# Kernel tuning notes

Measured on AMD Instinct MI355X. Metric: run time of the kernel, lower is better.

The kernel has to match this reference:

```python
import jax, jax.numpy as jnp
import numpy as np

# RT-DETR multi-scale deformable attention reference (PPMSDeformableAttention forward, value_mask=None)
SPATIAL_SHAPES = ((80, 80), (40, 40), (20, 20))  # (H, W) per level; sum(H*W) = 8400 = Len_v
NUM_HEADS = 8
NUM_LEVELS = 3
NUM_POINTS = 4


def _gather_corner(v_l, ix, iy, H, W):
    # v_l: [bs, heads, H*W, hd]; ix/iy: [bs, heads, N] int32 pixel indices (possibly out of range)
    valid = (ix >= 0) & (ix < W) & (iy >= 0) & (iy < H)
    idx = jnp.clip(iy, 0, H - 1) * W + jnp.clip(ix, 0, W - 1)
    g = jnp.take_along_axis(v_l, idx[..., None], axis=2)  # [bs, heads, N, hd]
    return jnp.where(valid[..., None], g, jnp.zeros((), v_l.dtype))


def _bilinear_sample(v_l, px, py, H, W):
    # grid_sample(align_corners=False, padding_mode='zeros') semantics.
    # v_l: [bs, heads, H*W, hd]; px/py: [bs, heads, N] continuous pixel coords
    x0 = jnp.floor(px).astype(jnp.int32)
    y0 = jnp.floor(py).astype(jnp.int32)
    x1, y1 = x0 + 1, y0 + 1
    wx1 = px - x0.astype(px.dtype)
    wy1 = py - y0.astype(py.dtype)
    wx0, wy0 = 1.0 - wx1, 1.0 - wy1
    out = (_gather_corner(v_l, x0, y0, H, W) * (wx0 * wy0)[..., None]
           + _gather_corner(v_l, x1, y0, H, W) * (wx1 * wy0)[..., None]
           + _gather_corner(v_l, x0, y1, H, W) * (wx0 * wy1)[..., None]
           + _gather_corner(v_l, x1, y1, H, W) * (wx1 * wy1)[..., None])
    return out  # [bs, heads, N, hd]


def setup_inputs() -> dict:
    key = jax.random.key(0)
    ks = jax.random.split(key, 8)
    bs, Lq, C = 32, 300, 256
    Lv = sum(h * w for h, w in SPATIAL_SHAPES)
    tp = NUM_HEADS * NUM_LEVELS * NUM_POINTS  # 96
    s = 1.0 / np.sqrt(C)
    return {
        "query": jax.random.normal(ks[0], (bs, Lq, C), jnp.float32),
        "reference_points": jax.random.uniform(ks[1], (bs, Lq, NUM_LEVELS, 4), jnp.float32, 0.05, 0.95),
        "value": jax.random.normal(ks[2], (bs, Lv, C), jnp.float32),
        "Wv": jax.random.normal(ks[3], (C, C), jnp.float32) * s,
        "bv": jnp.zeros((C,), jnp.float32),
        "Woff": jax.random.normal(ks[4], (C, tp * 2), jnp.float32) * (s * 0.1),
        "boff": jax.random.normal(ks[5], (tp * 2,), jnp.float32) * 0.5,
        "Watt": jax.random.normal(ks[6], (C, tp), jnp.float32) * s,
        "batt": jnp.zeros((tp,), jnp.float32),
        "Wout": jax.random.normal(ks[7], (C, C), jnp.float32) * s,
        "bout": jnp.zeros((C,), jnp.float32),
    }


def reference(query, reference_points, value, Wv, bv, Woff, boff, Watt, batt, Wout, bout):
    bs, Lq, C = query.shape
    H_, L, P = NUM_HEADS, NUM_LEVELS, NUM_POINTS
    hd = C // H_
    Lv = value.shape[1]

    # value projection -> [bs, heads, Lv, hd]
    v = (value @ Wv + bv).reshape(bs, Lv, H_, hd).transpose(0, 2, 1, 3)

    # sampling offsets and attention weights from query
    off = (query @ Woff + boff).reshape(bs, Lq, H_, L, P, 2)
    attw = jax.nn.softmax((query @ Watt + batt).reshape(bs, Lq, H_, L * P), axis=-1)
    attw = attw.reshape(bs, Lq, H_, L, P)

    # reference_points last dim == 4: (cx, cy, w, h) normalized
    ref_xy = reference_points[:, :, None, :, None, :2]  # [bs,Lq,1,L,1,2]
    ref_wh = reference_points[:, :, None, :, None, 2:]
    loc = ref_xy + off / P * ref_wh * 0.5  # [bs,Lq,H,L,P,2], normalized [0,1]

    out = jnp.zeros((bs, Lq, H_, hd), query.dtype)
    start = 0
    for l, (H, W) in enumerate(SPATIAL_SHAPES):
        v_l = v[:, :, start:start + H * W]  # [bs, heads, H*W, hd]
        start += H * W
        # normalized -> pixel coords (align_corners=False): p = loc * size - 0.5
        locl = loc[:, :, :, l]  # [bs, Lq, heads, P, 2]
        px = locl[..., 0] * W - 0.5
        py = locl[..., 1] * H - 0.5
        # [bs, Lq, heads, P] -> [bs, heads, Lq*P]
        px = px.transpose(0, 2, 1, 3).reshape(bs, H_, Lq * P)
        py = py.transpose(0, 2, 1, 3).reshape(bs, H_, Lq * P)
        sampled = _bilinear_sample(v_l, px, py, H, W)  # [bs, heads, Lq*P, hd]
        sampled = sampled.reshape(bs, H_, Lq, P, hd)
        out = out + jnp.einsum('bhqpd,bqhp->bqhd', sampled, attw[:, :, :, l])

    out = out.reshape(bs, Lq, C)
    return out @ Wout + bout
```

## Files before the change

### kernel.cpp

```cpp
#include <hip/hip_runtime.h>
#include <hip/hip_bf16.h>

#define BS 32
#define LQ 300
#define CDIM 256
#define HEADS 8
#define HD 32
#define NLEVELS 3
#define NPOINTS 4
#define LV 8400
#define NOA 288

typedef __attribute__((ext_vector_type(4))) float f32x4;
typedef __attribute__((ext_vector_type(8))) short short8;
typedef __attribute__((ext_vector_type(8))) unsigned short u16x8;
typedef __attribute__((ext_vector_type(4))) unsigned short u16x4;

__device__ __forceinline__ unsigned short f2bf(float f) {
    __hip_bfloat16 h = __float2bfloat16(f);
    return __bfloat16_as_ushort(h);
}
__device__ __forceinline__ float bf2f(unsigned short u) {
    union { unsigned u; float f; } v; v.u = ((unsigned)u) << 16;
    return v.f;
}

__global__ void prep_weights_kernel(
    const float* __restrict__ Wv, const float* __restrict__ Wout,
    const float* __restrict__ Woff, const float* __restrict__ Watt,
    unsigned short* __restrict__ WvT, unsigned short* __restrict__ WoutT,
    unsigned short* __restrict__ WoaT)
{
    const int bid = blockIdx.x;
    const int k = threadIdx.x;
    if (bid < 256) {
        WvT[bid * 256 + k] = f2bf(Wv[k * 256 + bid]);
    } else if (bid < 512) {
        const int n = bid - 256;
        WoutT[n * 256 + k] = f2bf(Wout[k * 256 + n]);
    } else {
        const int n = bid - 512;
        const float w = (n < 192) ? Woff[k * 192 + n] : Watt[k * 96 + (n - 192)];
        WoaT[n * 256 + k] = f2bf(w);
    }
}

#define BM 128
#define BK 32
#define PAD 40
#define EPAD 264
#define NT (CDIM / BK)

__global__ __launch_bounds__(512) void proj_value_mfma(
    const float* __restrict__ value, const unsigned short* __restrict__ WvT,
    const float* __restrict__ bv, unsigned short* __restrict__ vout)
{
    __shared__ alignas(16) unsigned short lds_w[2][256 * PAD];
    __shared__ alignas(16) unsigned short lds_x[2][128 * PAD];
    unsigned short* lds_ep = &lds_w[0][0];

    const int tid = threadIdx.x;
    const int lane = tid & 63;
    const int wave = tid >> 6;
    const int wm = wave >> 2;
    const int wn = wave & 3;
    const long row0 = (long)blockIdx.x * BM;

    const int wr = tid >> 1, wk = (tid & 1) * 16;
    const unsigned short* wptr = WvT + (size_t)wr * CDIM + wk;
    const int xr = tid >> 2, xk = (tid & 3) * 8;
    const float* xptr = value + (row0 + xr) * CDIM + xk;

    u16x8 wrg[2];
    f32x4 xrg[2];

    auto load_tile = [&](int kb) {
        const u16x8* qw = (const u16x8*)(wptr + kb);
        wrg[0] = qw[0]; wrg[1] = qw[1];
        const float* p = xptr + kb;
        xrg[0] = *(const f32x4*)(p);
        xrg[1] = *(const f32x4*)(p + 4);
    };
    auto write_tile = [&](int buf) {
        u16x8* ww = (u16x8*)&lds_w[buf][wr * PAD + wk];
        ww[0] = wrg[0]; ww[1] = wrg[1];
        u16x8 t0;
#pragma unroll
        for (int i = 0; i < 4; ++i) {
            t0[i]     = f2bf(xrg[0][i]);
            t0[i + 4] = f2bf(xrg[1][i]);
        }
        *(u16x8*)&lds_x[buf][xr * PAD + xk] = t0;
    };

    f32x4 acc[4][4] = {};
    const int la = lane & 15;
    const int lg = lane >> 4;

    load_tile(0);
    write_tile(0);
    __syncthreads();
    int cur = 0;

    for (int t = 0; t < NT; ++t) {
        if (t + 1 < NT) load_tile((t + 1) * BK);

        const unsigned short* pw = &lds_w[cur][(wn * 64 + la) * PAD + lg * 8];
        const unsigned short* px = &lds_x[cur][(wm * 64 + la) * PAD + lg * 8];
        short8 xf[4];
#pragma unroll
        for (int mf = 0; mf < 4; ++mf)
            xf[mf] = *(const short8*)(px + mf * 16 * PAD);
#pragma unroll
        for (int nf = 0; nf < 4; ++nf) {
            const short8 wf = *(const short8*)(pw + nf * 16 * PAD);
#pragma unroll
            for (int mf = 0; mf < 4; ++mf)
                acc[nf][mf] = __builtin_amdgcn_mfma_f32_16x16x32_bf16(wf, xf[mf], acc[nf][mf], 0, 0, 0);
        }

        if (t + 1 < NT) write_tile(cur ^ 1);
        __syncthreads();
        cur ^= 1;
    }

#pragma unroll
    for (int pass = 0; pass < 2; ++pass) {
        __syncthreads();
        if (wm == pass) {
#pragma unroll
            for (int nf = 0; nf < 4; ++nf) {
                const int nbase = wn * 64 + nf * 16 + lg * 4;
                const f32x4 bb = *(const f32x4*)&bv[nbase];
#pragma unroll
                for (int mf = 0; mf < 4; ++mf) {
                    const int mloc = mf * 16 + la;
                    u16x4 o;
#pragma unroll
                    for (int j = 0; j < 4; ++j) o[j] = f2bf(acc[nf][mf][j] + bb[j]);
                    *(u16x4*)&lds_ep[mloc * EPAD + nbase] = o;
                }
            }
        }
        __syncthreads();
        const int er = tid >> 3;
        const int ec = (tid & 7) * 32;
        const long gr = row0 + pass * 64 + er;
        const u16x8* src = (const u16x8*)&lds_ep[er * EPAD + ec];
        u16x8* dst = (u16x8*)&vout[gr * CDIM + ec];
#pragma unroll
        for (int i = 0; i < 4; ++i) dst[i] = src[i];
    }
}

#define APAD 40
#define BPAD 40

__global__ __launch_bounds__(256) void offatt_gemm_mfma(
    const float* __restrict__ query, const unsigned short* __restrict__ WoaT,
    const float* __restrict__ boff, const float* __restrict__ batt,
    float* __restrict__ offatt)
{
    __shared__ unsigned short lds_a[2][BM * APAD];
    __shared__ unsigned short lds_b[2][NOA * BPAD];

    const int tid = threadIdx.x;
    const int lane = tid & 63;
    const int wave = tid >> 6;
    const int wm = wave >> 1;
    const int wn = wave & 1;
    const long row0 = (long)blockIdx.x * BM;

    const int ar = tid >> 1;
    const int ak = (tid & 1) * 16;
    const float* aptr = query + (row0 + ar) * CDIM + ak;
    const unsigned short* bptr  = WoaT + (size_t)tid * CDIM;
    const unsigned short* bptr2 = WoaT + (size_t)(256 + tid) * CDIM;
    const bool extra = tid < 32;

    f32x4 arg[4];
    u16x8 brg[4], brg2[4];

    auto load_tile = [&](int kb) {
        const float* p = aptr + kb;
        arg[0] = *(const f32x4*)(p);
        arg[1] = *(const f32x4*)(p + 4);
        arg[2] = *(const f32x4*)(p + 8);
        arg[3] = *(const f32x4*)(p + 12);
        const u16x8* q = (const u16x8*)(bptr + kb);
        brg[0] = q[0]; brg[1] = q[1]; brg[2] = q[2]; brg[3] = q[3];
        if (extra) {
            const u16x8* q2 = (const u16x8*)(bptr2 + kb);
            brg2[0] = q2[0]; brg2[1] = q2[1]; brg2[2] = q2[2]; brg2[3] = q2[3];
        }
    };
    auto write_tile = [&](int buf) {
        u16x8 t0, t1;
#pragma unroll
        for (int i = 0; i < 4; ++i) {
            t0[i]     = f2bf(arg[0][i]);
            t0[i + 4] = f2bf(arg[1][i]);
            t1[i]     = f2bf(arg[2][i]);
            t1[i + 4] = f2bf(arg[3][i]);
        }
        u16x8* wa = (u16x8*)&lds_a[buf][ar * APAD + ak];
        wa[0] = t0; wa[1] = t1;
        u16x8* wb = (u16x8*)&lds_b[buf][tid * BPAD];
        wb[0] = brg[0]; wb[1] = brg[1]; wb[2] = brg[2]; wb[3] = brg[3];
        if (extra) {
            u16x8* wb2 = (u16x8*)&lds_b[buf][(256 + tid) * BPAD];
            wb2[0] = brg2[0]; wb2[1] = brg2[1]; wb2[2] = brg2[2]; wb2[3] = brg2[3];
        }
    };

    f32x4 acc[4][9] = {};
    const int la = lane & 15;
    const int lg = lane >> 4;

    load_tile(0);
    write_tile(0);
    __syncthreads();
    int cur = 0;

    for (int t = 0; t < CDIM / BK; ++t) {
        if (t + 1 < CDIM / BK) load_tile((t + 1) * BK);

        const unsigned short* pa = &lds_a[cur][(wm * 64 + la) * APAD + lg * 8];
        const unsigned short* pb = &lds_b[cur][(wn * 144 + la) * BPAD + lg * 8];
        short8 af[4];
#pragma unroll
        for (int mi = 0; mi < 4; ++mi)
            af[mi] = *(const short8*)(pa + mi * 16 * APAD);
#pragma unroll
        for (int ni = 0; ni < 9; ++ni) {
            const short8 bf = *(const short8*)(pb + ni * 16 * BPAD);
#pragma unroll
            for (int mi = 0; mi < 4; ++mi)
                acc[mi][ni] = __builtin_amdgcn_mfma_f32_16x16x32_bf16(af[mi], bf, acc[mi][ni], 0, 0, 0);
        }

        if (t + 1 < CDIM / BK) write_tile(cur ^ 1);
        __syncthreads();
        cur ^= 1;
    }

    float bias[9];
#pragma unroll
    for (int ni = 0; ni < 9; ++ni) {
        const int col = wn * 144 + ni * 16 + la;
        bias[ni] = (col < 192) ? boff[col] : batt[col - 192];
    }
#pragma unroll
    for (int mi = 0; mi < 4; ++mi) {
#pragma unroll
        for (int ni = 0; ni < 9; ++ni) {
            const int col = wn * 144 + ni * 16 + la;
#pragma unroll
            for (int j = 0; j < 4; ++j) {
                const long r = row0 + wm * 64 + mi * 16 + lg * 4 + j;
                offatt[r * NOA + col] = acc[mi][ni][j] + bias[ni];
            }
        }
    }
}

__global__ __launch_bounds__(256) void sample_kernel(
    const float* __restrict__ offatt, const float* __restrict__ refpts,
    const unsigned short* __restrict__ v, unsigned short* __restrict__ mid)
{
    __shared__ float oa_s[NOA];
    __shared__ float aw_s[96];
    __shared__ float px_s[96];
    __shared__ float py_s[96];

    const int tid = threadIdx.x;
    const int b = blockIdx.x / LQ;
    const int q = blockIdx.x % LQ;
    const long bq = (long)b * LQ + q;

    oa_s[tid] = offatt[bq * NOA + tid];
    if (tid < 32) oa_s[256 + tid] = offatt[bq * NOA + 256 + tid];
    __syncthreads();

    if (tid < 8) {
        float m = -1e30f;
#pragma unroll
        for (int i = 0; i < 12; ++i) m = fmaxf(m, oa_s[192 + tid * 12 + i]);
        float e[12];
        float s = 0.f;
#pragma unroll
        for (int i = 0; i < 12; ++i) { e[i] = __expf(oa_s[192 + tid * 12 + i] - m); s += e[i]; }
        const float inv = 1.f / s;
#pragma unroll
        for (int i = 0; i < 12; ++i) aw_s[tid * 12 + i] = e[i] * inv;
    }
    if (tid >= 128 && tid < 224) {
        const int t = tid - 128;
        const int h = t / 12, idx = t % 12, l = idx >> 2, p = idx & 3;
        const float* rp = refpts + (bq * NLEVELS + l) * 4;
        const float rx = rp[0], ry = rp[1], rw = rp[2], rh = rp[3];
        const float ox = oa_s[((h * NLEVELS + l) * NPOINTS + p) * 2 + 0];
        const float oy = oa_s[((h * NLEVELS + l) * NPOINTS + p) * 2 + 1];
        const float lx = rx + ox * 0.125f * rw;
        const float ly = ry + oy * 0.125f * rh;
        const int Wl = 80 >> l;
        px_s[t] = lx * (float)Wl - 0.5f;
        py_s[t] = ly * (float)Wl - 0.5f;
    }
    __syncthreads();

    const int h = tid >> 5;
    const int pg = (tid >> 3) & 3;
    const int d4 = tid & 7;
    const unsigned short* vb = v + ((size_t)b * LV) * CDIM + h * HD + d4 * 4;

    float a0 = 0.f, a1 = 0.f, a2 = 0.f, a3 = 0.f;
#pragma unroll
    for (int j = 0; j < 3; ++j) {
        const int i = pg * 3 + j;
        const int l = i >> 2;
        const int idx = h * 12 + i;
        const float px = px_s[idx], py = py_s[idx], aw = aw_s[idx];
        const int Wl = 80 >> l;
        const int start = (l == 0) ? 0 : (l == 1) ? 6400 : 8000;

        const float fx = floorf(px), fy = floorf(py);
        const int x0 = (int)fx, y0 = (int)fy;
        const float wx1 = px - fx, wy1 = py - fy;
        const float wx0 = 1.f - wx1, wy0 = 1.f - wy1;
        const float w00 = wx0 * wy0 * aw, w10 = wx1 * wy0 * aw;
        const float w01 = wx0 * wy1 * aw, w11 = wx1 * wy1 * aw;
        const bool x0v = (unsigned)x0 < (unsigned)Wl;
        const bool x1v = (unsigned)(x0 + 1) < (unsigned)Wl;
        const bool y0v = (unsigned)y0 < (unsigned)Wl;
        const bool y1v = (unsigned)(y0 + 1) < (unsigned)Wl;

        const unsigned short* base = vb + (size_t)start * CDIM;
        if (y0v) {
            const unsigned short* r0p = base + (size_t)(y0 * Wl) * CDIM;
            if (x0v) {
                const u16x4 u = *(const u16x4*)(r0p + (size_t)x0 * CDIM);
                a0 = fmaf(w00, bf2f(u[0]), a0); a1 = fmaf(w00, bf2f(u[1]), a1);
                a2 = fmaf(w00, bf2f(u[2]), a2); a3 = fmaf(w00, bf2f(u[3]), a3);
            }
            if (x1v) {
                const u16x4 u = *(const u16x4*)(r0p + (size_t)(x0 + 1) * CDIM);
                a0 = fmaf(w10, bf2f(u[0]), a0); a1 = fmaf(w10, bf2f(u[1]), a1);
                a2 = fmaf(w10, bf2f(u[2]), a2); a3 = fmaf(w10, bf2f(u[3]), a3);
            }
        }
        if (y1v) {
            const unsigned short* r1p = base + (size_t)((y0 + 1) * Wl) * CDIM;
            if (x0v) {
                const u16x4 u = *(const u16x4*)(r1p + (size_t)x0 * CDIM);
                a0 = fmaf(w01, bf2f(u[0]), a0); a1 = fmaf(w01, bf2f(u[1]), a1);
                a2 = fmaf(w01, bf2f(u[2]), a2); a3 = fmaf(w01, bf2f(u[3]), a3);
            }
            if (x1v) {
                const u16x4 u = *(const u16x4*)(r1p + (size_t)(x0 + 1) * CDIM);
                a0 = fmaf(w11, bf2f(u[0]), a0); a1 = fmaf(w11, bf2f(u[1]), a1);
                a2 = fmaf(w11, bf2f(u[2]), a2); a3 = fmaf(w11, bf2f(u[3]), a3);
            }
        }
    }

    a0 += __shfl_xor(a0, 8);  a1 += __shfl_xor(a1, 8);
    a2 += __shfl_xor(a2, 8);  a3 += __shfl_xor(a3, 8);
    a0 += __shfl_xor(a0, 16); a1 += __shfl_xor(a1, 16);
    a2 += __shfl_xor(a2, 16); a3 += __shfl_xor(a3, 16);

    if (pg == 0) {
        u16x4 o;
        o[0] = f2bf(a0); o[1] = f2bf(a1); o[2] = f2bf(a2); o[3] = f2bf(a3);
        *(u16x4*)&mid[bq * CDIM + h * HD + d4 * 4] = o;
    }
}

__global__ __launch_bounds__(256) void out_gemm_mfma(
    const unsigned short* __restrict__ mid, const unsigned short* __restrict__ WoutT,
    const float* __restrict__ bout, float* __restrict__ out)
{
    __shared__ unsigned short lds_w[2][256 * APAD];
    __shared__ unsigned short lds_x[2][BM * BPAD];

    const int tid = threadIdx.x;
    const int lane = tid & 63;
    const int wave = tid >> 6;
    const int wn = wave & 1;
    const int wm = wave >> 1;
    const long row0 = (long)blockIdx.x * BM;

    const unsigned short* wptr = WoutT + (size_t)tid * CDIM;
    const int xr = tid >> 1;
    const int xk = (tid & 1) * 16;
    const unsigned short* xptr = mid + (row0 + xr) * CDIM + xk;

    u16x8 wrg[4];
    u16x8 xrg[2];

    auto load_tile = [&](int kb) {
        const u16x8* qw = (const u16x8*)(wptr + kb);
        wrg[0] = qw[0]; wrg[1] = qw[1]; wrg[2] = qw[2]; wrg[3] = qw[3];
        const u16x8* qx = (const u16x8*)(xptr + kb);
        xrg[0] = qx[0]; xrg[1] = qx[1];
    };
    auto write_tile = [&](int buf) {
        u16x8* ww = (u16x8*)&lds_w[buf][tid * APAD];
        ww[0] = wrg[0]; ww[1] = wrg[1]; ww[2] = wrg[2]; ww[3] = wrg[3];
        u16x8* wx = (u16x8*)&lds_x[buf][xr * BPAD + xk];
        wx[0] = xrg[0]; wx[1] = xrg[1];
    };

    f32x4 acc[8][4] = {};
    const int la = lane & 15;
    const int lg = lane >> 4;

    load_tile(0);
    write_tile(0);
    __syncthreads();
    int cur = 0;

    for (int t = 0; t < CDIM / BK; ++t) {
        if (t + 1 < CDIM / BK) load_tile((t + 1) * BK);

        const unsigned short* pw = &lds_w[cur][(wn * 128 + la) * APAD + lg * 8];
        const unsigned short* px = &lds_x[cur][(wm * 64 + la) * BPAD + lg * 8];
        short8 xf[4];
#pragma unroll
        for (int mf = 0; mf < 4; ++mf)
            xf[mf] = *(const short8*)(px + mf * 16 * BPAD);
#pragma unroll
        for (int nf = 0; nf < 8; ++nf) {
            const short8 wf = *(const short8*)(pw + nf * 16 * APAD);
#pragma unroll
            for (int mf = 0; mf < 4; ++mf)
                acc[nf][mf] = __builtin_amdgcn_mfma_f32_16x16x32_bf16(wf, xf[mf], acc[nf][mf], 0, 0, 0);
        }

        if (t + 1 < CDIM / BK) write_tile(cur ^ 1);
        __syncthreads();
        cur ^= 1;
    }

#pragma unroll
    for (int nf = 0; nf < 8; ++nf) {
        const int nbase = wn * 128 + nf * 16 + lg * 4;
        const f32x4 bb = *(const f32x4*)&bout[nbase];
#pragma unroll
        for (int mf = 0; mf < 4; ++mf) {
            const long m = row0 + wm * 64 + mf * 16 + la;
            f32x4 o;
#pragma unroll
            for (int j = 0; j < 4; ++j) o[j] = acc[nf][mf][j] + bb[j];
            *(f32x4*)&out[m * CDIM + nbase] = o;
        }
    }
}

extern "C" void kernel_launch(void* const* d_in, const int* in_sizes, int n_in,
                              void* d_out, int out_size, void* d_ws, size_t ws_size,
                              hipStream_t stream) {
    const float* query = (const float*)d_in[0];
    const float* refp  = (const float*)d_in[1];
    const float* value = (const float*)d_in[2];
    const float* Wv    = (const float*)d_in[3];
    const float* bv    = (const float*)d_in[4];
    const float* Woff  = (const float*)d_in[5];
    const float* boff  = (const float*)d_in[6];
    const float* Watt  = (const float*)d_in[7];
    const float* batt  = (const float*)d_in[8];
    const float* Wout  = (const float*)d_in[9];
    const float* bout  = (const float*)d_in[10];
    float* out = (float*)d_out;

    char* ws = (char*)d_ws;
    unsigned short* v = (unsigned short*)ws;
    size_t off = (size_t)BS * LV * CDIM * 2;
    float* offatt = (float*)(ws + off);
    off += (size_t)BS * LQ * NOA * 4;
    unsigned short* mid = (unsigned short*)(ws + off);
    off += (size_t)BS * LQ * CDIM * 2;
    unsigned short* WvT = (unsigned short*)(ws + off);
    off += 256 * 256 * 2;
    unsigned short* WoaT = (unsigned short*)(ws + off);
    off += NOA * 256 * 2;
    unsigned short* WoutT = (unsigned short*)(ws + off);

    prep_weights_kernel<<<800, 256, 0, stream>>>(Wv, Wout, Woff, Watt, WvT, WoutT, WoaT);
    proj_value_mfma<<<(BS * LV) / BM, 512, 0, stream>>>(value, WvT, bv, v);
    offatt_gemm_mfma<<<(BS * LQ) / BM, 256, 0, stream>>>(query, WoaT, boff, batt, offatt);
    sample_kernel<<<BS * LQ, 256, 0, stream>>>(offatt, refp, v, mid);
    out_gemm_mfma<<<(BS * LQ) / BM, 256, 0, stream>>>(mid, WoutT, bout, out);
}
```

Before: 213.4 us.

## Shrink value-projection tile to 64 rows and interleave sample blocks across batches

The value projection GEMM now uses 64-row tiles with 256 threads. Each of the four waves covers 64 output columns across all 64 rows, and the two-pass epilogue collapses into a single pass. This doubles the grid and cuts LDS per block, aiming for better occupancy and latency hiding, at the cost of reloading the weight tile for twice as many blocks. The sample kernel also remaps block indices so that consecutive blocks visit 8 different batches at the same query, which changes the order in which the value gather touches L2/cache.

```diff
diff --git a/kernel.cpp b/kernel.cpp
--- a/kernel.cpp
+++ b/kernel.cpp
@@ -46,44 +46,44 @@
 }
 
 #define BM 128
+#define BMP 64
 #define BK 32
 #define PAD 40
 #define EPAD 264
 #define NT (CDIM / BK)
 
-__global__ __launch_bounds__(512) void proj_value_mfma(
+__global__ __launch_bounds__(256) void proj_value_mfma(
     const float* __restrict__ value, const unsigned short* __restrict__ WvT,
     const float* __restrict__ bv, unsigned short* __restrict__ vout)
 {
     __shared__ alignas(16) unsigned short lds_w[2][256 * PAD];
-    __shared__ alignas(16) unsigned short lds_x[2][128 * PAD];
+    __shared__ alignas(16) unsigned short lds_x[2][BMP * PAD];
     unsigned short* lds_ep = &lds_w[0][0];
 
     const int tid = threadIdx.x;
     const int lane = tid & 63;
     const int wave = tid >> 6;
-    const int wm = wave >> 2;
-    const int wn = wave & 3;
-    const long row0 = (long)blockIdx.x * BM;
-
-    const int wr = tid >> 1, wk = (tid & 1) * 16;
-    const unsigned short* wptr = WvT + (size_t)wr * CDIM + wk;
+    const long row0 = (long)blockIdx.x * BMP;
+    const int la = lane & 15;
+    const int lg = lane >> 4;
+
+    const unsigned short* wptr = WvT + (size_t)tid * CDIM;
     const int xr = tid >> 2, xk = (tid & 3) * 8;
     const float* xptr = value + (row0 + xr) * CDIM + xk;
 
-    u16x8 wrg[2];
+    u16x8 wrg[4];
     f32x4 xrg[2];
 
     auto load_tile = [&](int kb) {
         const u16x8* qw = (const u16x8*)(wptr + kb);
-        wrg[0] = qw[0]; wrg[1] = qw[1];
+        wrg[0] = qw[0]; wrg[1] = qw[1]; wrg[2] = qw[2]; wrg[3] = qw[3];
         const float* p = xptr + kb;
         xrg[0] = *(const f32x4*)(p);
         xrg[1] = *(const f32x4*)(p + 4);
     };
     auto write_tile = [&](int buf) {
-        u16x8* ww = (u16x8*)&lds_w[buf][wr * PAD + wk];
-        ww[0] = wrg[0]; ww[1] = wrg[1];
+        u16x8* ww = (u16x8*)&lds_w[buf][tid * PAD];
+        ww[0] = wrg[0]; ww[1] = wrg[1]; ww[2] = wrg[2]; ww[3] = wrg[3];
         u16x8 t0;
 #pragma unroll
         for (int i = 0; i < 4; ++i) {
@@ -94,8 +94,6 @@
     };
 
     f32x4 acc[4][4] = {};
-    const int la = lane & 15;
-    const int lg = lane >> 4;
 
     load_tile(0);
     write_tile(0);
@@ -105,8 +103,8 @@
     for (int t = 0; t < NT; ++t) {
         if (t + 1 < NT) load_tile((t + 1) * BK);
 
-        const unsigned short* pw = &lds_w[cur][(wn * 64 + la) * PAD + lg * 8];
-        const unsigned short* px = &lds_x[cur][(wm * 64 + la) * PAD + lg * 8];
+        const unsigned short* pw = &lds_w[cur][(wave * 64 + la) * PAD + lg * 8];
+        const unsigned short* px = &lds_x[cur][la * PAD + lg * 8];
         short8 xf[4];
 #pragma unroll
         for (int mf = 0; mf < 4; ++mf)
@@ -125,32 +123,26 @@
     }
 
 #pragma unroll
-    for (int pass = 0; pass < 2; ++pass) {
-        __syncthreads();
-        if (wm == pass) {
-#pragma unroll
-            for (int nf = 0; nf < 4; ++nf) {
-                const int nbase = wn * 64 + nf * 16 + lg * 4;
-                const f32x4 bb = *(const f32x4*)&bv[nbase];
-#pragma unroll
-                for (int mf = 0; mf < 4; ++mf) {
-                    const int mloc = mf * 16 + la;
-                    u16x4 o;
-#pragma unroll
-                    for (int j = 0; j < 4; ++j) o[j] = f2bf(acc[nf][mf][j] + bb[j]);
-                    *(u16x4*)&lds_ep[mloc * EPAD + nbase] = o;
-                }
-            }
-        }
-        __syncthreads();
-        const int er = tid >> 3;
-        const int ec = (tid & 7) * 32;
-        const long gr = row0 + pass * 64 + er;
-        const u16x8* src = (const u16x8*)&lds_ep[er * EPAD + ec];
-        u16x8* dst = (u16x8*)&vout[gr * CDIM + ec];
-#pragma unroll
-        for (int i = 0; i < 4; ++i) dst[i] = src[i];
-    }
+    for (int nf = 0; nf < 4; ++nf) {
+        const int nbase = wave * 64 + nf * 16 + lg * 4;
+        const f32x4 bb = *(const f32x4*)&bv[nbase];
+#pragma unroll
+        for (int mf = 0; mf < 4; ++mf) {
+            const int mloc = mf * 16 + la;
+            u16x4 o;
+#pragma unroll
+            for (int j = 0; j < 4; ++j) o[j] = f2bf(acc[nf][mf][j] + bb[j]);
+            *(u16x4*)&lds_ep[mloc * EPAD + nbase] = o;
+        }
+    }
+    __syncthreads();
+    const int er = tid >> 2;
+    const int ec = (tid & 3) * 64;
+    const long gr = row0 + er;
+    const u16x8* src = (const u16x8*)&lds_ep[er * EPAD + ec];
+    u16x8* dst = (u16x8*)&vout[gr * CDIM + ec];
+#pragma unroll
+    for (int i = 0; i < 8; ++i) dst[i] = src[i];
 }
 
 #define APAD 40
@@ -274,8 +266,12 @@
     __shared__ float py_s[96];
 
     const int tid = threadIdx.x;
-    const int b = blockIdx.x / LQ;
-    const int q = blockIdx.x % LQ;
+    const int nb = blockIdx.x;
+    const int x = nb & 7;
+    const int rest = nb >> 3;
+    const int g = rest / LQ;
+    const int q = rest % LQ;
+    const int b = g * 8 + x;
     const long bq = (long)b * LQ + q;
 
     oa_s[tid] = offatt[bq * NOA + tid];
@@ -487,7 +483,7 @@
     unsigned short* WoutT = (unsigned short*)(ws + off);
 
     prep_weights_kernel<<<800, 256, 0, stream>>>(Wv, Wout, Woff, Watt, WvT, WoutT, WoaT);
-    proj_value_mfma<<<(BS * LV) / BM, 512, 0, stream>>>(value, WvT, bv, v);
+    proj_value_mfma<<<(BS * LV) / BMP, 256, 0, stream>>>(value, WvT, bv, v);
     offatt_gemm_mfma<<<(BS * LQ) / BM, 256, 0, stream>>>(query, WoaT, boff, batt, offatt);
     sample_kernel<<<BS * LQ, 256, 0, stream>>>(offatt, refp, v, mid);
     out_gemm_mfma<<<(BS * LQ) / BM, 256, 0, stream>>>(mid, WoutT, bout, out);
```

Result: slower. 230.4 us (+8.0%).

## Stage value-projection tiles via direct global-to-LDS loads and remap sampling blocks per XCD

Applied to the files above, without the earlier changes.

The value-projection GEMM now issues 16-byte global_load_lds transfers straight into XOR-swizzled LDS tiles, replacing the register round-trip. Activations are kept in fp32 in LDS and converted to bf16 when fragments are read. This is meant to cut register pressure and VALU work in the load path, and to overlap the next tile's fetch with the MFMA loop, at the cost of twice the LDS footprint for the activation tile. Separately, the sampling kernel remaps block indices so that consecutive blocks come from 8 different batches. Each XCD should then mostly touch one batch's value tensor, which improves L2 locality for the gathers.

```diff
diff --git a/kernel.cpp b/kernel.cpp
--- a/kernel.cpp
+++ b/kernel.cpp
@@ -23,6 +23,17 @@
 __device__ __forceinline__ float bf2f(unsigned short u) {
     union { unsigned u; float f; } v; v.u = ((unsigned)u) << 16;
     return v.f;
+}
+__device__ __forceinline__ short8 cvt8(const f32x4 a, const f32x4 b) {
+    u16x8 c;
+#pragma unroll
+    for (int i = 0; i < 4; ++i) { c[i] = f2bf(a[i]); c[i + 4] = f2bf(b[i]); }
+    union { u16x8 u; short8 s; } v; v.u = c; return v.s;
+}
+__device__ __forceinline__ void gload16(const void* g, void* l) {
+    __builtin_amdgcn_global_load_lds(
+        (const __attribute__((address_space(1))) void*)g,
+        (__attribute__((address_space(3))) void*)l, 16, 0, 0);
 }
 
 __global__ void prep_weights_kernel(
@@ -47,7 +58,6 @@
 
 #define BM 128
 #define BK 32
-#define PAD 40
 #define EPAD 264
 #define NT (CDIM / BK)
 
@@ -55,78 +65,76 @@
     const float* __restrict__ value, const unsigned short* __restrict__ WvT,
     const float* __restrict__ bv, unsigned short* __restrict__ vout)
 {
-    __shared__ alignas(16) unsigned short lds_w[2][256 * PAD];
-    __shared__ alignas(16) unsigned short lds_x[2][128 * PAD];
-    unsigned short* lds_ep = &lds_w[0][0];
+    __shared__ alignas(16) char lds_raw[65536];
+    unsigned short* lds_w = (unsigned short*)lds_raw;
+    float* lds_x = (float*)(lds_raw + 32768);
+    unsigned short* lds_ep = (unsigned short*)lds_raw;
 
     const int tid = threadIdx.x;
     const int lane = tid & 63;
     const int wave = tid >> 6;
+    const int wn = wave & 3;
     const int wm = wave >> 2;
-    const int wn = wave & 3;
     const long row0 = (long)blockIdx.x * BM;
-
-    const int wr = tid >> 1, wk = (tid & 1) * 16;
-    const unsigned short* wptr = WvT + (size_t)wr * CDIM + wk;
-    const int xr = tid >> 2, xk = (tid & 3) * 8;
-    const float* xptr = value + (row0 + xr) * CDIM + xk;
-
-    u16x8 wrg[2];
-    f32x4 xrg[2];
-
-    auto load_tile = [&](int kb) {
-        const u16x8* qw = (const u16x8*)(wptr + kb);
-        wrg[0] = qw[0]; wrg[1] = qw[1];
-        const float* p = xptr + kb;
-        xrg[0] = *(const f32x4*)(p);
-        xrg[1] = *(const f32x4*)(p + 4);
-    };
-    auto write_tile = [&](int buf) {
-        u16x8* ww = (u16x8*)&lds_w[buf][wr * PAD + wk];
-        ww[0] = wrg[0]; ww[1] = wrg[1];
-        u16x8 t0;
-#pragma unroll
-        for (int i = 0; i < 4; ++i) {
-            t0[i]     = f2bf(xrg[0][i]);
-            t0[i + 4] = f2bf(xrg[1][i]);
-        }
-        *(u16x8*)&lds_x[buf][xr * PAD + xk] = t0;
-    };
-
-    f32x4 acc[4][4] = {};
     const int la = lane & 15;
     const int lg = lane >> 4;
 
-    load_tile(0);
-    write_tile(0);
-    __syncthreads();
+    const int widx0 = tid;
+    const int wrd0 = widx0 >> 2, wqd0 = widx0 & 3;
+    const int wrd1 = (512 + tid) >> 2, wqd1 = (512 + tid) & 3;
+    const unsigned short* wsrc0 = WvT + (size_t)wrd0 * CDIM + (wqd0 ^ (wrd0 & 3)) * 8;
+    const unsigned short* wsrc1 = WvT + (size_t)wrd1 * CDIM + (wqd1 ^ (wrd1 & 3)) * 8;
+    const int xrd0 = tid >> 3, xqd0 = tid & 7;
+    const int xrd1 = (512 + tid) >> 3, xqd1 = (512 + tid) & 7;
+    const float* xsrc0 = value + (row0 + xrd0) * (long)CDIM + (xqd0 ^ (xrd0 & 7)) * 4;
+    const float* xsrc1 = value + (row0 + xrd1) * (long)CDIM + (xqd1 ^ (xrd1 & 7)) * 4;
+    const int wavebase = (tid & ~63) * 8;
+
+    auto stage = [&](int buf, int kb) {
+        unsigned short* wb = lds_w + buf * (256 * 32);
+        gload16(wsrc0 + kb, wb + wavebase);
+        gload16(wsrc1 + kb, wb + 512 * 8 + wavebase);
+        float* xb = lds_x + buf * (128 * 32);
+        gload16(xsrc0 + kb, (unsigned short*)xb + wavebase);
+        gload16(xsrc1 + kb, (unsigned short*)xb + 512 * 8 + wavebase);
+    };
+
+    f32x4 acc[4][4] = {};
+    const int wsw = la & 3;
+    const int xsw = la & 7;
+
+    stage(0, 0);
     int cur = 0;
 
     for (int t = 0; t < NT; ++t) {
-        if (t + 1 < NT) load_tile((t + 1) * BK);
-
-        const unsigned short* pw = &lds_w[cur][(wn * 64 + la) * PAD + lg * 8];
-        const unsigned short* px = &lds_x[cur][(wm * 64 + la) * PAD + lg * 8];
+        __syncthreads();
+        if (t + 1 < NT) stage(cur ^ 1, (t + 1) * BK);
+
+        const unsigned short* wbuf = lds_w + cur * (256 * 32);
+        const float* xbuf = lds_x + cur * (128 * 32);
         short8 xf[4];
 #pragma unroll
-        for (int mf = 0; mf < 4; ++mf)
-            xf[mf] = *(const short8*)(px + mf * 16 * PAD);
+        for (int mf = 0; mf < 4; ++mf) {
+            const float* px = xbuf + (wm * 64 + mf * 16 + la) * 32;
+            const f32x4 a = *(const f32x4*)(px + ((2 * lg + 0) ^ xsw) * 4);
+            const f32x4 b = *(const f32x4*)(px + ((2 * lg + 1) ^ xsw) * 4);
+            xf[mf] = cvt8(a, b);
+        }
 #pragma unroll
         for (int nf = 0; nf < 4; ++nf) {
-            const short8 wf = *(const short8*)(pw + nf * 16 * PAD);
+            const unsigned short* pw = wbuf + (wn * 64 + nf * 16 + la) * 32;
+            const short8 wf = *(const short8*)(pw + (lg ^ wsw) * 8);
 #pragma unroll
             for (int mf = 0; mf < 4; ++mf)
                 acc[nf][mf] = __builtin_amdgcn_mfma_f32_16x16x32_bf16(wf, xf[mf], acc[nf][mf], 0, 0, 0);
         }
-
-        if (t + 1 < NT) write_tile(cur ^ 1);
-        __syncthreads();
         cur ^= 1;
     }
 
+    __syncthreads();
 #pragma unroll
     for (int pass = 0; pass < 2; ++pass) {
-        __syncthreads();
+        if (pass) __syncthreads();
         if (wm == pass) {
 #pragma unroll
             for (int nf = 0; nf < 4; ++nf) {
@@ -274,8 +282,12 @@
     __shared__ float py_s[96];
 
     const int tid = threadIdx.x;
-    const int b = blockIdx.x / LQ;
-    const int q = blockIdx.x % LQ;
+    const int nb = blockIdx.x;
+    const int x = nb & 7;
+    const int rest = nb >> 3;
+    const int g = rest / LQ;
+    const int q = rest % LQ;
+    const int b = g * 8 + x;
     const long bq = (long)b * LQ + q;
 
     oa_s[tid] = offatt[bq * NOA + tid];
```

Measured after the change: 213.5 us. Within noise of the previous version (+0.0%).
